# Kernel optimization log

Measured on AMD Instinct MI355X. Metric: run time of the kernel, lower is better.

## Reference

```python
import jax, jax.numpy as jnp
import numpy as np

MARGIN = 1.0

def _safe_sqrt(x):
    # sqrt with zero gradient at x<=0 (matches relu().sqrt() forward; avoids NaN grads on the zero diagonal)
    pos = x > 0
    return jnp.where(pos, jnp.sqrt(jnp.where(pos, x, 1.0)), 0.0)

def _smoothed_metric_loss(X, m=MARGIN):
    # X: [N, d], N even; lifted-structure smoothed loss (Song et al.)
    N = X.shape[0]
    sq = jnp.sum(X * X, axis=1)                       # [N]
    G = X @ X.T                                       # [N, N]
    D = _safe_sqrt(jax.nn.relu(sq[:, None] + sq[None, :] - 2.0 * G))
    E = jnp.exp(m - D)                                # [N, N]
    P = N // 2
    i = jnp.arange(P) * 2
    j = i + 1
    # negatives for pair p: rows {i,j}, all cols except {i,j}
    row_pair_sum = E.reshape(P, 2, N).sum(axis=(1, 2))  # [P] = rowsum(i)+rowsum(j)
    excl = E[i, i] + E[i, j] + E[j, i] + E[j, j]
    neg_sum = row_pair_sum - excl
    J = jnp.log(neg_sum) + D[i, j]
    return jnp.sum(jax.nn.relu(J) ** 2) / (2.0 * P)

def reference(text_embeddings, shape_embeddings):
    N = text_embeddings.shape[0]
    # tt loss on text embeddings
    metric_tt = _smoothed_metric_loss(text_embeddings, MARGIN)
    # repeat each shape embedding twice (index_select with i//2)
    shape_rep = jnp.repeat(shape_embeddings, 2, axis=0)  # [N, d]
    mask = jnp.tile(jnp.array([1.0, 0.0], dtype=text_embeddings.dtype), N // 2)[:, None]
    inv = 1.0 - mask
    e1 = text_embeddings * mask + shape_rep * inv
    e2 = text_embeddings * inv + shape_rep * mask
    emb = jnp.concatenate([e1, e2], axis=0)              # [2N, d]
    metric_st = _smoothed_metric_loss(emb, MARGIN)
    return metric_tt + metric_st

def setup_inputs() -> dict:
    key = jax.random.key(0)
    k1, k2 = jax.random.split(key)
    N, Dim = 4096, 256
    text = jax.random.normal(k1, (N, Dim), dtype=jnp.float32)
    shape = jax.random.normal(k2, (N // 2, Dim), dtype=jnp.float32)
    return {"text_embeddings": text, "shape_embeddings": shape}
```

## Files before the change

### kernel.cpp

```cpp
#include <hip/hip_runtime.h>
#include <hip/hip_bf16.h>
#include <math.h>


typedef __bf16 bf16x8 __attribute__((ext_vector_type(8)));
typedef float floatx4 __attribute__((ext_vector_type(4)));

#define KD 256
#define NU 6144
#define NBU 48
#define TU (NBU * (NBU + 1) / 2)
#define BM 128
#define BK 32
#define ECONST 2.718281828459045f

#define LSLOT(r, q) ((((r) * 4 + ((q) ^ (((r) >> 1) & 3)))) * 8)

__device__ __forceinline__ void gload_lds16(const void* g, void* l) {
  __builtin_amdgcn_global_load_lds((const __attribute__((address_space(1))) unsigned int*)g,
                                   (__attribute__((address_space(3))) unsigned int*)l,
                                   16, 0, 0);
}

__global__ __launch_bounds__(256) void prep_kernel(const float* __restrict__ text,
                                                   const float* __restrict__ shape,
                                                   __bf16* __restrict__ Xu,
                                                   float* __restrict__ sq,
                                                   float* __restrict__ rowacc,
                                                   float* __restrict__ out, int out_n) {
  int gt = blockIdx.x * 256 + threadIdx.x;
  if (gt < 2 * NU) rowacc[gt] = 0.f;
  if (gt < out_n) out[gt] = 0.f;
  int wave = gt >> 6;
  int lane = gt & 63;
  const float* src = (wave < 4096) ? (text + (size_t)wave * KD)
                                   : (shape + (size_t)(wave - 4096) * KD);
  __bf16* dst = Xu + (size_t)wave * KD;
  float s = 0.f;
#pragma unroll
  for (int j = 0; j < 4; ++j) {
    int idx = j * 64 + lane;
    float f = src[idx];
    __bf16 h = (__bf16)f;
    dst[idx] = h;
    float fv = (float)h;
    s += fv * fv;
  }
#pragma unroll
  for (int m = 1; m < 64; m <<= 1) s += __shfl_xor(s, m, 64);
  if (lane == 0) sq[wave] = s;
}

__global__ __launch_bounds__(256, 3) void egemm_tri_kernel(
    const __bf16* __restrict__ X, const float* __restrict__ sq,
    float* __restrict__ rowacc) {
  __shared__ __align__(16) __bf16 As[BM * BK];
  __shared__ __align__(16) __bf16 Bs[BM * BK];
  __shared__ float rowbuf[2][128];
  __shared__ float colbuf[2][128];

  int t = blockIdx.x;
  int by = (int)((sqrtf(8.0f * (float)t + 1.0f) - 1.0f) * 0.5f);
  while ((by + 1) * (by + 2) / 2 <= t) ++by;
  while (by * (by + 1) / 2 > t) --by;
  const int bx = t - by * (by + 1) / 2;

  const int mBase = by * BM;
  const int nBase = bx * BM;
  const bool diag = (by == bx);

  const int tid = threadIdx.x;
  const int lane = tid & 63;
  const int w = tid >> 6;
  const int warpM = w >> 1, warpN = w & 1;
  const int quad = lane >> 4;
  const int l15 = lane & 15;

  floatx4 acc[4][4] = {};

  const int sRow = lane >> 2;
  const int sCol = (((lane & 3) ^ ((lane >> 3) & 3))) * 8;

  for (int kt = 0; kt < KD; kt += BK) {
    __syncthreads();
#pragma unroll
    for (int h = 0; h < 2; ++h) {
      int c = h * 4 + w;
      gload_lds16(X + (size_t)(mBase + c * 16 + sRow) * KD + kt + sCol, &As[c * 512]);
      gload_lds16(X + (size_t)(nBase + c * 16 + sRow) * KD + kt + sCol, &Bs[c * 512]);
    }
    __syncthreads();

    bf16x8 af[4], bfr[4];
#pragma unroll
    for (int tm = 0; tm < 4; ++tm)
      af[tm] = *(const bf16x8*)&As[LSLOT(warpM * 64 + tm * 16 + l15, quad)];
#pragma unroll
    for (int tn = 0; tn < 4; ++tn)
      bfr[tn] = *(const bf16x8*)&Bs[LSLOT(warpN * 64 + tn * 16 + l15, quad)];
#pragma unroll
    for (int tm = 0; tm < 4; ++tm)
#pragma unroll
      for (int tn = 0; tn < 4; ++tn)
        acc[tm][tn] = __builtin_amdgcn_mfma_f32_16x16x32_bf16(af[tm], bfr[tn], acc[tm][tn], 0, 0, 0);
  }

  const int rbase = mBase + warpM * 64;
  const int cbase = nBase + warpN * 64;
  float sqr[4][4], sqc[4];
#pragma unroll
  for (int tm = 0; tm < 4; ++tm)
#pragma unroll
    for (int r = 0; r < 4; ++r)
      sqr[tm][r] = sq[rbase + tm * 16 + quad * 4 + r];
#pragma unroll
  for (int tn = 0; tn < 4; ++tn)
    sqc[tn] = sq[cbase + tn * 16 + l15];

  const float L2E = 1.44269504088896f;
  float cs[4] = {0.f, 0.f, 0.f, 0.f};
#pragma unroll
  for (int tm = 0; tm < 4; ++tm) {
    float rs[4] = {0.f, 0.f, 0.f, 0.f};
#pragma unroll
    for (int tn = 0; tn < 4; ++tn) {
#pragma unroll
      for (int r = 0; r < 4; ++r) {
        float v = acc[tm][tn][r];
        float dsq = fmaf(-2.0f, v, sqr[tm][r] + sqc[tn]);
        float dst = sqrtf(fmaxf(dsq, 0.f));
        float ev = __builtin_amdgcn_exp2f(fmaf(-L2E, dst, L2E));
        if (diag && tm == tn && (quad * 4 + r) == l15) ev = 0.f;
        rs[r] += ev;
        cs[tn] += ev;
      }
    }
#pragma unroll
    for (int r = 0; r < 4; ++r) {
      float v = rs[r];
      v += __shfl_xor(v, 1, 64);
      v += __shfl_xor(v, 2, 64);
      v += __shfl_xor(v, 4, 64);
      v += __shfl_xor(v, 8, 64);
      if (l15 == 0) rowbuf[warpN][warpM * 64 + tm * 16 + quad * 4 + r] = v;
    }
  }
#pragma unroll
  for (int tn = 0; tn < 4; ++tn) {
    float v = cs[tn];
    v += __shfl_xor(v, 16, 64);
    v += __shfl_xor(v, 32, 64);
    if (quad == 0) colbuf[warpM][warpN * 64 + tn * 16 + l15] = v;
  }
  __syncthreads();

  float* rdst = rowacc + (bx < 32 ? 0 : NU);
  float* cdst = rowacc + (by < 32 ? 0 : NU);
  if (tid < 128) {
    atomicAdd(&rdst[mBase + tid], rowbuf[0][tid] + rowbuf[1][tid]);
  } else if (!diag) {
    int c = tid - 128;
    atomicAdd(&cdst[nBase + c], colbuf[0][c] + colbuf[1][c]);
  }
}

__global__ __launch_bounds__(256) void loss_kernel(const float* __restrict__ text,
                                                   const float* __restrict__ shape,
                                                   const float* __restrict__ rowacc,
                                                   float* __restrict__ out) {
  __shared__ float part[4];
  const float* St = rowacc;
  const float* Ss = rowacc + NU;
  const int w = threadIdx.x >> 6;
  const int lane = threadIdx.x & 63;
  float jacc = 0.f;
#pragma unroll
  for (int it = 0; it < 2; ++it) {
    int wv = it * 3072 + blockIdx.x * 4 + w;
    const float *a, *b;
    float base, scale;
    if (wv < 2048) {
      int p = wv;
      a = text + (size_t)(2 * p) * KD;
      b = text + (size_t)(2 * p + 1) * KD;
      base = St[2 * p] + St[2 * p + 1];
      scale = 1.0f / 4096.0f;
    } else {
      int p = wv - 2048;
      int u1, u2;
      if (p < 2048) {
        u1 = 2 * p; u2 = 4096 + p;
        a = text + (size_t)(2 * p) * KD;
        b = shape + (size_t)p * KD;
      } else {
        int s = p - 2048;
        u1 = 4096 + s; u2 = 2 * s + 1;
        a = shape + (size_t)s * KD;
        b = text + (size_t)(2 * s + 1) * KD;
      }
      float g1 = St[u1] + 2.0f * Ss[u1];
      float g2 = St[u2] + 2.0f * Ss[u2];
      base = g1 + g2 + ECONST;
      scale = 1.0f / 8192.0f;
    }
    float s = 0.f;
#pragma unroll
    for (int j = 0; j < 4; ++j) {
      int idx = j * 64 + lane;
      float d = a[idx] - b[idx];
      s += d * d;
    }
#pragma unroll
    for (int m = 1; m < 64; m <<= 1) s += __shfl_xor(s, m, 64);
    if (lane == 0) {
      float D = s > 0.f ? sqrtf(s) : 0.f;
      float ns = base - 2.0f * expf(1.0f - D);
      float J = logf(ns) + D;
      jacc += (J > 0.f) ? J * J * scale : 0.f;
    }
  }
  if (lane == 0) part[w] = jacc;
  __syncthreads();
  if (threadIdx.x == 0) atomicAdd(out, part[0] + part[1] + part[2] + part[3]);
}

extern "C" void kernel_launch(void* const* d_in, const int* in_sizes, int n_in,
                              void* d_out, int out_size, void* d_ws, size_t ws_size,
                              hipStream_t stream) {
  const float* text = (const float*)d_in[0];
  const float* shape = (const float*)d_in[1];
  float* out = (float*)d_out;

  char* ws = (char*)d_ws;
  __bf16* Xu = (__bf16*)ws;
  float* sq = (float*)(ws + (size_t)NU * KD * 2);
  float* rowacc = sq + NU;

  prep_kernel<<<NU / 4, 256, 0, stream>>>(text, shape, Xu, sq, rowacc, out, out_size);
  egemm_tri_kernel<<<TU, 256, 0, stream>>>(Xu, sq, rowacc);
  loss_kernel<<<768, 256, 0, stream>>>(text, shape, rowacc, out);
}
```

Measured before the change: 99.59 us.

## Double-buffer LDS tiles in the GEMM and vectorize loads in prep and loss kernels

The triangular GEMM kernel now keeps two LDS buffers, prefetching the next K tile with direct global-to-LDS loads while MFMAs run on the current one. This replaces the two barriers per K step with one waitcnt plus one barrier. The prep and loss kernels switch from scalar strided loads to float4 loads per lane, and the prep kernel writes packed bf16 pairs. LDS use doubles, which may limit occupancy under the 3-blocks-per-CU launch bound.

```diff
diff --git a/kernel.cpp b/kernel.cpp
--- a/kernel.cpp
+++ b/kernel.cpp
@@ -35,17 +35,14 @@
   int lane = gt & 63;
   const float* src = (wave < 4096) ? (text + (size_t)wave * KD)
                                    : (shape + (size_t)(wave - 4096) * KD);
-  __bf16* dst = Xu + (size_t)wave * KD;
-  float s = 0.f;
-#pragma unroll
-  for (int j = 0; j < 4; ++j) {
-    int idx = j * 64 + lane;
-    float f = src[idx];
-    __bf16 h = (__bf16)f;
-    dst[idx] = h;
-    float fv = (float)h;
-    s += fv * fv;
-  }
+  float4 v = ((const float4*)src)[lane];
+  __bf16 h0 = (__bf16)v.x, h1 = (__bf16)v.y, h2 = (__bf16)v.z, h3 = (__bf16)v.w;
+  union { __bf16 h[4]; ushort2 u2[2]; } pk;
+  pk.h[0] = h0; pk.h[1] = h1; pk.h[2] = h2; pk.h[3] = h3;
+  ((ushort2*)(Xu + (size_t)wave * KD))[lane * 2] = pk.u2[0];
+  ((ushort2*)(Xu + (size_t)wave * KD))[lane * 2 + 1] = pk.u2[1];
+  float f0 = (float)h0, f1 = (float)h1, f2 = (float)h2, f3 = (float)h3;
+  float s = f0 * f0 + f1 * f1 + f2 * f2 + f3 * f3;
 #pragma unroll
   for (int m = 1; m < 64; m <<= 1) s += __shfl_xor(s, m, 64);
   if (lane == 0) sq[wave] = s;
@@ -54,8 +51,8 @@
 __global__ __launch_bounds__(256, 3) void egemm_tri_kernel(
     const __bf16* __restrict__ X, const float* __restrict__ sq,
     float* __restrict__ rowacc) {
-  __shared__ __align__(16) __bf16 As[BM * BK];
-  __shared__ __align__(16) __bf16 Bs[BM * BK];
+  __shared__ __align__(16) __bf16 As[2][BM * BK];
+  __shared__ __align__(16) __bf16 Bs[2][BM * BK];
   __shared__ float rowbuf[2][128];
   __shared__ float colbuf[2][128];
 
@@ -81,29 +78,39 @@
   const int sRow = lane >> 2;
   const int sCol = (((lane & 3) ^ ((lane >> 3) & 3))) * 8;
 
-  for (int kt = 0; kt < KD; kt += BK) {
-    __syncthreads();
-#pragma unroll
-    for (int h = 0; h < 2; ++h) {
-      int c = h * 4 + w;
-      gload_lds16(X + (size_t)(mBase + c * 16 + sRow) * KD + kt + sCol, &As[c * 512]);
-      gload_lds16(X + (size_t)(nBase + c * 16 + sRow) * KD + kt + sCol, &Bs[c * 512]);
-    }
-    __syncthreads();
+#define STAGE(b, kt)                                                                   \
+  {                                                                                    \
+    _Pragma("unroll") for (int h = 0; h < 2; ++h) {                                    \
+      int c = h * 4 + w;                                                               \
+      gload_lds16(X + (size_t)(mBase + c * 16 + sRow) * KD + (kt) + sCol,              \
+                  &As[b][c * 512]);                                                    \
+      gload_lds16(X + (size_t)(nBase + c * 16 + sRow) * KD + (kt) + sCol,              \
+                  &Bs[b][c * 512]);                                                    \
+    }                                                                                  \
+  }
+
+  STAGE(0, 0);
+  for (int it = 0; it < KD / BK; ++it) {
+    const int cur = it & 1;
+    asm volatile("s_waitcnt vmcnt(0)" ::: "memory");
+    __builtin_amdgcn_s_barrier();
+    asm volatile("" ::: "memory");
+    if (it < KD / BK - 1) STAGE(cur ^ 1, (it + 1) * BK);
 
     bf16x8 af[4], bfr[4];
 #pragma unroll
     for (int tm = 0; tm < 4; ++tm)
-      af[tm] = *(const bf16x8*)&As[LSLOT(warpM * 64 + tm * 16 + l15, quad)];
+      af[tm] = *(const bf16x8*)&As[cur][LSLOT(warpM * 64 + tm * 16 + l15, quad)];
 #pragma unroll
     for (int tn = 0; tn < 4; ++tn)
-      bfr[tn] = *(const bf16x8*)&Bs[LSLOT(warpN * 64 + tn * 16 + l15, quad)];
+      bfr[tn] = *(const bf16x8*)&Bs[cur][LSLOT(warpN * 64 + tn * 16 + l15, quad)];
 #pragma unroll
     for (int tm = 0; tm < 4; ++tm)
 #pragma unroll
       for (int tn = 0; tn < 4; ++tn)
         acc[tm][tn] = __builtin_amdgcn_mfma_f32_16x16x32_bf16(af[tm], bfr[tn], acc[tm][tn], 0, 0, 0);
   }
+#undef STAGE
 
   const int rbase = mBase + warpM * 64;
   const int cbase = nBase + warpN * 64;
@@ -203,13 +210,10 @@
       base = g1 + g2 + ECONST;
       scale = 1.0f / 8192.0f;
     }
-    float s = 0.f;
-#pragma unroll
-    for (int j = 0; j < 4; ++j) {
-      int idx = j * 64 + lane;
-      float d = a[idx] - b[idx];
-      s += d * d;
-    }
+    float4 va = ((const float4*)a)[lane];
+    float4 vb = ((const float4*)b)[lane];
+    float d0 = va.x - vb.x, d1 = va.y - vb.y, d2 = va.z - vb.z, d3 = va.w - vb.w;
+    float s = d0 * d0 + d1 * d1 + d2 * d2 + d3 * d3;
 #pragma unroll
     for (int m = 1; m < 64; m <<= 1) s += __shfl_xor(s, m, 64);
     if (lane == 0) {
```

After: 101.4 us. No clear change (+1.8%).
